# Kernel tuning notes

Measured on AMD Instinct MI355X. Metric: run time of the kernel, lower is better.

## Reference

```python
import jax, jax.numpy as jnp
import numpy as np

N_USERS = 200000
N_MOVIES = 80000
N = N_USERS + N_MOVIES
H = 64
F_MOVIE = 20
E = 1250000
EL = 500000


def setup_inputs() -> dict:
    key = jax.random.key(0)
    ks = jax.random.split(key, 13)
    s = 0.05
    inp = {
        "movie_x": jax.random.normal(ks[0], (N_MOVIES, F_MOVIE), jnp.float32),
        "user_emb": jax.random.normal(ks[1], (N_USERS, H), jnp.float32) * s,
        "movie_emb": jax.random.normal(ks[2], (N_MOVIES, H), jnp.float32) * s,
        "lin_W": jax.random.normal(ks[3], (H, F_MOVIE), jnp.float32) * s,
        "lin_b": jax.random.normal(ks[4], (H,), jnp.float32) * s,
        "W1l": jax.random.normal(ks[5], (H, H), jnp.float32) * s,
        "b1": jax.random.normal(ks[6], (H,), jnp.float32) * s,
        "W1r": jax.random.normal(ks[7], (H, H), jnp.float32) * s,
        "W2l": jax.random.normal(ks[8], (H, H), jnp.float32) * s,
        "b2": jax.random.normal(ks[9], (H,), jnp.float32) * s,
        "W2r": jax.random.normal(ks[10], (H, H), jnp.float32) * s,
        "edge_index": jax.random.randint(ks[11], (2, E), 0, N, jnp.int64),
        "edge_label_index": jnp.stack([
            jax.random.randint(jax.random.fold_in(ks[12], 0), (EL,), 0, N_USERS, jnp.int64),
            jax.random.randint(jax.random.fold_in(ks[12], 1), (EL,), 0, N_MOVIES, jnp.int64),
        ]),
    }
    return inp


def _sage(x, src, dst, Wl, bl, Wr):
    # PyG SAGEConv, mean aggregation: lin_l(mean_{j->i} x_j) + lin_r(x_i)
    msg = x[src]  # [E, H] gather
    agg = jax.ops.segment_sum(msg, dst, num_segments=N)  # [N, H] scatter-add
    deg = jax.ops.segment_sum(jnp.ones((src.shape[0],), x.dtype), dst, num_segments=N)
    mean = agg / jnp.maximum(deg, 1.0)[:, None]
    return mean @ Wl.T + bl + x @ Wr.T


def reference(movie_x, user_emb, movie_emb, lin_W, lin_b,
              W1l, b1, W1r, W2l, b2, W2r, edge_index, edge_label_index):
    # encode: users = embedding lookup (node_id == arange), movies = linear(x) + embedding
    x_user = user_emb
    x_movie = movie_x @ lin_W.T + lin_b + movie_emb
    x = jnp.concatenate([x_user, x_movie], axis=0)  # [N, H]

    src, dst = edge_index[0], edge_index[1]
    x = jax.nn.relu(_sage(x, src, dst, W1l, b1, W1r))
    x = _sage(x, src, dst, W2l, b2, W2r)

    xu = x[:N_USERS]
    xm = x[N_USERS:]
    # dot-product edge scoring over supervision edges
    u = xu[edge_label_index[0]]  # [EL, H]
    m = xm[edge_label_index[1]]  # [EL, H]
    return jnp.sum(u * m, axis=-1)  # [EL]
```

## Files before the change

kernel.cpp:

```cpp
#include <hip/hip_runtime.h>
#include <hip/hip_bf16.h>

#define NU 200000
#define NM 80000
#define NT 280000
#define HD 64
#define FM 20

#define BSHIFT 10
#define NBUCK ((NT + 1023) >> 10)
#define SCHUNK 4096

typedef __attribute__((ext_vector_type(8))) short short8;
typedef __attribute__((ext_vector_type(4))) float floatx4;

__device__ __forceinline__ float bfu2f(unsigned short u) {
    union { unsigned int u; float f; } c; c.u = ((unsigned int)u) << 16; return c.f;
}

__device__ __forceinline__ unsigned short f2bf_raw(float f) {
    union { float f; unsigned int u; } c; c.f = f;
    unsigned int u = c.u + 0x7FFFu + ((c.u >> 16) & 1u);
    return (unsigned short)(u >> 16);
}

__device__ __forceinline__ float ldf(const void* p, long i, int isbf) {
    return isbf ? bfu2f(((const unsigned short*)p)[i]) : ((const float*)p)[i];
}
__device__ __forceinline__ int ldidx(const int* p, long j, int is64) {
    return is64 ? p[2 * j] : p[j];
}

__global__ void probe_kernel(const void* user_emb, const int* ei, int* flags) {
    int t = threadIdx.x;
    int bad = 0;
    for (int i = t; i < 128; i += 64) {
        unsigned short h = ((const unsigned short*)user_emb)[i];
        unsigned int e = (h >> 7) & 0xFF;
        if (e >= 135) bad = 1;
    }
    unsigned long long mf = __ballot(bad != 0);
    int odd_nonzero = 0;
    if (t < 16 && ei[2 * t + 1] != 0) odd_nonzero = 1;
    unsigned long long mi = __ballot(odd_nonzero != 0);
    if (t == 0) {
        flags[0] = (mf == 0) ? 1 : 0;
        flags[1] = (mi == 0) ? 1 : 0;
    }
}

__global__ __launch_bounds__(256) void prep_user(
    const void* __restrict__ user_emb,
    unsigned short* __restrict__ xb,
    const int* __restrict__ flags)
{
    long t = (long)blockIdx.x * 256 + threadIdx.x;
    int isbf = flags[0];
    if (isbf) {
        ((short8*)xb)[t] = ((const short8*)user_emb)[t];
    } else {
        floatx4 a = ((const floatx4*)user_emb)[2 * t];
        floatx4 b = ((const floatx4*)user_emb)[2 * t + 1];
        short8 r;
        r[0] = (short)f2bf_raw(a[0]); r[1] = (short)f2bf_raw(a[1]);
        r[2] = (short)f2bf_raw(a[2]); r[3] = (short)f2bf_raw(a[3]);
        r[4] = (short)f2bf_raw(b[0]); r[5] = (short)f2bf_raw(b[1]);
        r[6] = (short)f2bf_raw(b[2]); r[7] = (short)f2bf_raw(b[3]);
        ((short8*)xb)[t] = r;
    }
}

__global__ __launch_bounds__(256) void prep_movie(
    const void* __restrict__ movie_x,
    const void* __restrict__ movie_emb,
    const void* __restrict__ lin_W,
    const void* __restrict__ lin_b,
    unsigned short* __restrict__ xb,
    const int* __restrict__ flags)
{
    int isbf = flags[0];
    int tid = threadIdx.x;
    int lane = tid & 63;
    int wave = blockIdx.x * 4 + (tid >> 6);
    int m0 = __builtin_amdgcn_readfirstlane(wave << 2);
    if (m0 >= NM) return;

    float wr[FM];
    if (isbf) {
        const unsigned int* p = (const unsigned int*)((const unsigned short*)lin_W + (long)lane * FM);
        #pragma unroll
        for (int i = 0; i < FM / 2; ++i) {
            unsigned int u = p[i];
            wr[2 * i]     = bfu2f((unsigned short)(u & 0xFFFFu));
            wr[2 * i + 1] = bfu2f((unsigned short)(u >> 16));
        }
    } else {
        const floatx4* p = (const floatx4*)((const float*)lin_W + (long)lane * FM);
        #pragma unroll
        for (int i = 0; i < FM / 4; ++i) {
            floatx4 v = p[i];
            wr[4 * i] = v[0]; wr[4 * i + 1] = v[1]; wr[4 * i + 2] = v[2]; wr[4 * i + 3] = v[3];
        }
    }
    float bias = ldf(lin_b, lane, isbf);

    #pragma unroll
    for (int mm = 0; mm < 4; ++mm) {
        int m = m0 + mm;
        float a0 = bias + ldf(movie_emb, (long)m * HD + lane, isbf);
        float a1 = 0.f, a2 = 0.f, a3 = 0.f;
        if (isbf) {
            const unsigned int* mr = (const unsigned int*)((const unsigned short*)movie_x + (long)m * FM);
            #pragma unroll
            for (int kk = 0; kk < FM / 2; ++kk) {
                unsigned int u = mr[kk];
                float x0 = bfu2f((unsigned short)(u & 0xFFFFu));
                float x1 = bfu2f((unsigned short)(u >> 16));
                if (kk & 1) { a2 += x0 * wr[2 * kk]; a3 += x1 * wr[2 * kk + 1]; }
                else        { a0 += x0 * wr[2 * kk]; a1 += x1 * wr[2 * kk + 1]; }
            }
        } else {
            const float* mr = (const float*)movie_x + (long)m * FM;
            #pragma unroll
            for (int k = 0; k < FM; k += 4) {
                a0 += mr[k]     * wr[k];
                a1 += mr[k + 1] * wr[k + 1];
                a2 += mr[k + 2] * wr[k + 2];
                a3 += mr[k + 3] * wr[k + 3];
            }
        }
        xb[(long)(NU + m) * HD + lane] = f2bf_raw((a0 + a1) + (a2 + a3));
    }
}

__global__ __launch_bounds__(512) void blk_hist(
    const int* __restrict__ ei, int E,
    int* __restrict__ blkhist,
    const int* __restrict__ flags)
{
    __shared__ int h[NBUCK];
    int tid = threadIdx.x;
    for (int i = tid; i < NBUCK; i += 512) h[i] = 0;
    __syncthreads();
    int is64 = flags[1];
    long e0 = (long)blockIdx.x * SCHUNK;
    long e1 = e0 + SCHUNK; if (e1 > E) e1 = E;
    for (long j = e0 + tid; j < e1; j += 512) {
        int d = ldidx(ei, (long)E + j, is64);
        atomicAdd(&h[d >> BSHIFT], 1);
    }
    __syncthreads();
    long obase = (long)blockIdx.x * NBUCK;
    for (int i = tid; i < NBUCK; i += 512) blkhist[obase + i] = h[i];
}

__global__ __launch_bounds__(256) void col_scan(
    int* __restrict__ blkhist, int NSB,
    int* __restrict__ bcnt)
{
    __shared__ int larr[2048];
    __shared__ int lsum[256];
    int b = blockIdx.x;
    int t = threadIdx.x;
    for (int i = t; i < NSB; i += 256) larr[i] = blkhist[(long)i * NBUCK + b];
    __syncthreads();
    int C = (NSB + 255) >> 8;
    int beg = t * C;
    int end = beg + C; if (end > NSB) end = NSB; if (beg > NSB) beg = NSB;
    int s = 0;
    for (int i = beg; i < end; ++i) s += larr[i];
    lsum[t] = s;
    __syncthreads();
    for (int off = 1; off < 256; off <<= 1) {
        int v = lsum[t];
        if (t >= off) v += lsum[t - off];
        __syncthreads();
        lsum[t] = v;
        __syncthreads();
    }
    int run = (t == 0) ? 0 : lsum[t - 1];
    for (int i = beg; i < end; ++i) {
        int v = larr[i];
        blkhist[(long)i * NBUCK + b] = run;
        run += v;
    }
    if (t == 0) bcnt[b] = lsum[255];
}

__global__ __launch_bounds__(256) void bucket_scan(
    const int* __restrict__ bcnt, int* __restrict__ bstart, int E)
{
    __shared__ int s[256];
    int t = threadIdx.x;
    int a0 = (2 * t     < NBUCK) ? bcnt[2 * t]     : 0;
    int a1 = (2 * t + 1 < NBUCK) ? bcnt[2 * t + 1] : 0;
    s[t] = a0 + a1;
    __syncthreads();
    for (int off = 1; off < 256; off <<= 1) {
        int v = s[t];
        if (t >= off) v += s[t - off];
        __syncthreads();
        s[t] = v;
        __syncthreads();
    }
    int run = (t == 0) ? 0 : s[t - 1];
    if (2 * t     < NBUCK) bstart[2 * t]     = run;
    if (2 * t + 1 < NBUCK) bstart[2 * t + 1] = run + a0;
    if (t == 0) bstart[NBUCK] = E;
}

__global__ __launch_bounds__(512) void scatter_kernel(
    const int* __restrict__ ei, int E,
    const int* __restrict__ bstart,
    const int* __restrict__ blkhist,
    int* __restrict__ packed,
    const int* __restrict__ flags)
{
    __shared__ int cur[NBUCK];
    int tid = threadIdx.x;
    long obase = (long)blockIdx.x * NBUCK;
    for (int i = tid; i < NBUCK; i += 512) cur[i] = bstart[i] + blkhist[obase + i];
    __syncthreads();
    int is64 = flags[1];
    long e0 = (long)blockIdx.x * SCHUNK;
    long e1 = e0 + SCHUNK; if (e1 > E) e1 = E;
    for (long j = e0 + tid; j < e1; j += 512) {
        int s = ldidx(ei, j, is64);
        int d = ldidx(ei, (long)E + j, is64);
        int b = d >> BSHIFT;
        int pos = atomicAdd(&cur[b], 1);
        packed[pos] = (s << BSHIFT) | (d & ((1 << BSHIFT) - 1));
    }
}

__global__ __launch_bounds__(256) void finefill_kernel(
    const int* __restrict__ bstart,
    const int* __restrict__ packed,
    int* __restrict__ rowptr,
    int* __restrict__ cnt,
    int* __restrict__ srclist)
{
    __shared__ int lcnt[1 << BSHIFT];
    __shared__ int lsum[256];
    int b = blockIdx.x;
    int tid = threadIdx.x;
    int nbase = b << BSHIFT;
    int beg = bstart[b];
    int end = bstart[b + 1];

    for (int i = tid; i < (1 << BSHIFT); i += 256) lcnt[i] = 0;
    __syncthreads();

    for (int j = beg + tid; j < end; j += 256)
        atomicAdd(&lcnt[packed[j] & ((1 << BSHIFT) - 1)], 1);
    __syncthreads();

    int i0 = tid * 4;
    int c0 = lcnt[i0], c1 = lcnt[i0 + 1], c2 = lcnt[i0 + 2], c3 = lcnt[i0 + 3];
    lsum[tid] = c0 + c1 + c2 + c3;
    __syncthreads();
    for (int off = 1; off < 256; off <<= 1) {
        int v = lsum[tid];
        if (tid >= off) v += lsum[tid - off];
        __syncthreads();
        lsum[tid] = v;
        __syncthreads();
    }
    int run = beg + ((tid == 0) ? 0 : lsum[tid - 1]);
    int r0 = run, r1 = r0 + c0, r2 = r1 + c1, r3 = r2 + c2;

    int n0 = nbase + i0;
    if (n0     < NT) { rowptr[n0]     = r0; cnt[n0]     = c0; }
    if (n0 + 1 < NT) { rowptr[n0 + 1] = r1; cnt[n0 + 1] = c1; }
    if (n0 + 2 < NT) { rowptr[n0 + 2] = r2; cnt[n0 + 2] = c2; }
    if (n0 + 3 < NT) { rowptr[n0 + 3] = r3; cnt[n0 + 3] = c3; }

    lcnt[i0] = r0; lcnt[i0 + 1] = r1; lcnt[i0 + 2] = r2; lcnt[i0 + 3] = r3;
    __syncthreads();

    for (int j = beg + tid; j < end; j += 256) {
        int p = packed[j];
        int dl = p & ((1 << BSHIFT) - 1);
        int pos = atomicAdd(&lcnt[dl], 1);
        srclist[pos] = p >> BSHIFT;
    }
}

template <bool RELU>
__global__ __launch_bounds__(256) void sage_layer(
    const unsigned short* __restrict__ xin,
    const int* __restrict__ rowptr,
    const int* __restrict__ cnt,
    const int* __restrict__ srclist,
    const void* __restrict__ Wl,
    const void* __restrict__ bias,
    const void* __restrict__ Wr,
    unsigned short* __restrict__ xout,
    const int* __restrict__ flags)
{
    __shared__ short8 lWl8[HD * HD / 8];
    __shared__ short8 lWr8[HD * HD / 8];
    __shared__ short8 lmean8[HD * HD / 8];
    __shared__ float lb[HD];
    unsigned short* lWl  = (unsigned short*)lWl8;
    unsigned short* lWr  = (unsigned short*)lWr8;
    unsigned short* lm   = (unsigned short*)lmean8;

    int tid = threadIdx.x;
    int isbf = flags[0];

    if (isbf) {
        const short8* wl8 = (const short8*)Wl;
        const short8* wr8 = (const short8*)Wr;
        for (int i = tid; i < HD * HD / 8; i += 256) { lWl8[i] = wl8[i]; lWr8[i] = wr8[i]; }
    } else {
        const floatx4* wlf = (const floatx4*)Wl;
        const floatx4* wrf = (const floatx4*)Wr;
        for (int i = tid; i < HD * HD / 8; i += 256) {
            floatx4 a = wlf[2 * i], b = wlf[2 * i + 1];
            short8 r;
            r[0]=(short)f2bf_raw(a[0]); r[1]=(short)f2bf_raw(a[1]); r[2]=(short)f2bf_raw(a[2]); r[3]=(short)f2bf_raw(a[3]);
            r[4]=(short)f2bf_raw(b[0]); r[5]=(short)f2bf_raw(b[1]); r[6]=(short)f2bf_raw(b[2]); r[7]=(short)f2bf_raw(b[3]);
            lWl8[i] = r;
            a = wrf[2 * i]; b = wrf[2 * i + 1];
            r[0]=(short)f2bf_raw(a[0]); r[1]=(short)f2bf_raw(a[1]); r[2]=(short)f2bf_raw(a[2]); r[3]=(short)f2bf_raw(a[3]);
            r[4]=(short)f2bf_raw(b[0]); r[5]=(short)f2bf_raw(b[1]); r[6]=(short)f2bf_raw(b[2]); r[7]=(short)f2bf_raw(b[3]);
            lWr8[i] = r;
        }
    }
    if (tid < HD) lb[tid] = ldf(bias, tid, isbf);

    int tile = blockIdx.x;
    long base = (long)tile * HD * HD;

    int w = tid >> 6;
    int lane = tid & 63;
    int mrow = lane & 15;
    int quad = lane >> 4;

    const short8* xrow = (const short8*)&xin[base + (long)(w * 16 + mrow) * HD];
    short8 ax0 = xrow[quad];
    short8 ax1 = xrow[4 + quad];

    int g = lane >> 2;
    int sub = lane & 3;
    int nl = w * 16 + g;
    int n = tile * 64 + nl;
    int beg = rowptr[n];
    int deg = cnt[n];

    float acc[16];
    #pragma unroll
    for (int k = 0; k < 16; ++k) acc[k] = 0.f;

    for (int j0 = 0; j0 < deg; j0 += 4) {
        int e = j0 + sub;
        int sv = (e < deg) ? srclist[beg + e] : 0;
        int cq = deg - j0; if (cq > 4) cq = 4;
        short8 r[4][2];
        #pragma unroll
        for (int q = 0; q < 4; ++q) {
            int s = __shfl(sv, (g << 2) | q);
            const short8* p = (const short8*)&xin[(long)s * HD + sub * 16];
            r[q][0] = p[0];
            r[q][1] = p[1];
        }
        #pragma unroll
        for (int q = 0; q < 4; ++q) {
            if (q < cq) {
                #pragma unroll
                for (int k = 0; k < 8; ++k) {
                    acc[k]     += bfu2f((unsigned short)r[q][0][k]);
                    acc[k + 8] += bfu2f((unsigned short)r[q][1][k]);
                }
            }
        }
    }

    float rd = 1.0f / fmaxf((float)deg, 1.0f);
    short8 o0, o1;
    #pragma unroll
    for (int k = 0; k < 8; ++k) {
        o0[k] = (short)f2bf_raw(acc[k] * rd);
        o1[k] = (short)f2bf_raw(acc[k + 8] * rd);
    }
    *(short8*)&lm[nl * HD + sub * 16]     = o0;
    *(short8*)&lm[nl * HD + sub * 16 + 8] = o1;

    __syncthreads();

    short8 am0 = *(const short8*)&lm[(w * 16 + mrow) * HD + quad * 8];
    short8 am1 = *(const short8*)&lm[(w * 16 + mrow) * HD + 32 + quad * 8];

    floatx4 acc4[4];
    #pragma unroll
    for (int ht = 0; ht < 4; ++ht) {
        int h = ht * 16 + mrow;
        short8 bl0 = *(const short8*)&lWl[h * HD + quad * 8];
        short8 bl1 = *(const short8*)&lWl[h * HD + 32 + quad * 8];
        short8 br0 = *(const short8*)&lWr[h * HD + quad * 8];
        short8 br1 = *(const short8*)&lWr[h * HD + 32 + quad * 8];
        floatx4 a = {0.f, 0.f, 0.f, 0.f};
        a = __builtin_amdgcn_mfma_f32_16x16x32_bf16(am0, bl0, a, 0, 0, 0);
        a = __builtin_amdgcn_mfma_f32_16x16x32_bf16(am1, bl1, a, 0, 0, 0);
        a = __builtin_amdgcn_mfma_f32_16x16x32_bf16(ax0, br0, a, 0, 0, 0);
        a = __builtin_amdgcn_mfma_f32_16x16x32_bf16(ax1, br1, a, 0, 0, 0);
        acc4[ht] = a;
    }

    #pragma unroll
    for (int ht = 0; ht < 4; ++ht) {
        int h = ht * 16 + mrow;
        float bv = lb[h];
        #pragma unroll
        for (int r = 0; r < 4; ++r) {
            int node = w * 16 + quad * 4 + r;
            float v = acc4[ht][r] + bv;
            if (RELU) v = fmaxf(v, 0.0f);
            xout[base + node * HD + h] = f2bf_raw(v);
        }
    }
}

__global__ __launch_bounds__(256) void dot_kernel(
    const unsigned short* __restrict__ x2,
    const int* __restrict__ eli,
    void* __restrict__ out,
    int EL,
    const int* __restrict__ flags)
{
    int wid = (blockIdx.x * 256 + threadIdx.x) >> 6;
    long base = (long)wid * 16;
    if (base >= EL) return;
    int lane = threadIdx.x & 63;
    int isbf = flags[0];
    int is64 = flags[1];

    int idxv = 0;
    if (lane < 16)      idxv = ldidx(eli, base + lane, is64);
    else if (lane < 32) idxv = ldidx(eli, (long)EL + base + (lane - 16), is64);

    int e   = lane >> 2;
    int seg = lane & 3;
    int u = __shfl(idxv, e);
    int m = __shfl(idxv, 16 + e);

    const short8* up = (const short8*)(x2 + (long)u * HD + seg * 16);
    const short8* mp = (const short8*)(x2 + (long)(NU + m) * HD + seg * 16);
    short8 a0 = up[0], a1 = up[1];
    short8 b0 = mp[0], b1 = mp[1];

    float p = 0.f;
    #pragma unroll
    for (int j = 0; j < 8; ++j) {
        p += bfu2f((unsigned short)a0[j]) * bfu2f((unsigned short)b0[j]);
        p += bfu2f((unsigned short)a1[j]) * bfu2f((unsigned short)b1[j]);
    }
    p += __shfl_xor(p, 1);
    p += __shfl_xor(p, 2);

    if (seg == 0) {
        long g = base + e;
        if (isbf) ((unsigned short*)out)[g] = f2bf_raw(p);
        else      ((float*)out)[g] = p;
    }
}

extern "C" void kernel_launch(void* const* d_in, const int* in_sizes, int n_in,
                              void* d_out, int out_size, void* d_ws, size_t ws_size,
                              hipStream_t stream)
{
    const void* movie_x   = d_in[0];
    const void* user_emb  = d_in[1];
    const void* movie_emb = d_in[2];
    const void* lin_W     = d_in[3];
    const void* lin_b     = d_in[4];
    const void* W1l       = d_in[5];
    const void* b1        = d_in[6];
    const void* W1r       = d_in[7];
    const void* W2l       = d_in[8];
    const void* b2        = d_in[9];
    const void* W2r       = d_in[10];
    const int* ei  = (const int*)d_in[11];
    const int* eli = (const int*)d_in[12];
    int E  = in_sizes[11] / 2;
    int EL = in_sizes[12] / 2;

    const int NSB = (E + SCHUNK - 1) / SCHUNK;

    char* w = (char*)d_ws;
    unsigned short* xb0     = (unsigned short*)w;  w += (size_t)NT * HD * 2;
    unsigned short* xb1     = (unsigned short*)w;  w += (size_t)NT * HD * 2;
    int*            cnt     = (int*)w;             w += (size_t)NT * 4;
    int*            rowptr  = (int*)w;             w += (size_t)NT * 4;
    int*            srclist = (int*)w;             w += (size_t)E * 4;
    int*            packed  = (int*)w;             w += (size_t)E * 4;
    int*            bcnt    = (int*)w;             w += (size_t)(NBUCK + 1) * 4;
    int*            bstart  = (int*)w;             w += (size_t)(NBUCK + 1) * 4;
    int*            blkhist = (int*)w;             w += (size_t)NSB * NBUCK * 4;
    int*            flags   = (int*)w;

    const int user_blocks   = (NU * HD / 8) / 256;
    const int movie_blocks  = NM / 16;
    const int tile_blocks   = NT / 64;
    const int dot_blocks    = ((EL + 15) / 16 + 3) / 4;

    probe_kernel<<<1, 64, 0, stream>>>(user_emb, ei, flags);

    prep_user<<<user_blocks, 256, 0, stream>>>(user_emb, xb0, flags);
    prep_movie<<<movie_blocks, 256, 0, stream>>>(movie_x, movie_emb, lin_W, lin_b, xb0, flags);

    blk_hist<<<NSB, 512, 0, stream>>>(ei, E, blkhist, flags);
    col_scan<<<NBUCK, 256, 0, stream>>>(blkhist, NSB, bcnt);
    bucket_scan<<<1, 256, 0, stream>>>(bcnt, bstart, E);
    scatter_kernel<<<NSB, 512, 0, stream>>>(ei, E, bstart, blkhist, packed, flags);
    finefill_kernel<<<NBUCK, 256, 0, stream>>>(bstart, packed, rowptr, cnt, srclist);

    sage_layer<true><<<tile_blocks, 256, 0, stream>>>(xb0, rowptr, cnt, srclist, W1l, b1, W1r, xb1, flags);
    sage_layer<false><<<tile_blocks, 256, 0, stream>>>(xb1, rowptr, cnt, srclist, W2l, b2, W2r, xb0, flags);

    dot_kernel<<<dot_blocks, 256, 0, stream>>>(xb0, eli, d_out, EL, flags);
}
```

Measured before the change: 305.7 us.

## Widen SAGE layer to 512 threads with 8 lanes per node and padded LDS

The SAGE layer kernel now runs 512 threads per 64-node tile. Each node's neighbor gather is spread over 8 lanes, each loading 16 bytes per neighbor, and up to 8 neighbors are gathered per iteration. The MFMA output work is split so each wave computes two of the four 16-column tiles. Shared-memory rows for the weights and mean tile are padded to 72 elements to avoid LDS bank conflicts. The goals are more memory-level parallelism in the latency-bound gather and cheaper LDS reads, at the cost of larger blocks and redundant per-wave A-fragment loads.

```diff
diff --git a/kernel.cpp b/kernel.cpp
--- a/kernel.cpp
+++ b/kernel.cpp
@@ -10,6 +10,9 @@
 #define BSHIFT 10
 #define NBUCK ((NT + 1023) >> 10)
 #define SCHUNK 4096
+
+#define PD 72
+#define PD8 (PD / 8)
 
 typedef __attribute__((ext_vector_type(8))) short short8;
 typedef __attribute__((ext_vector_type(4))) float floatx4;
@@ -287,7 +290,7 @@
 }
 
 template <bool RELU>
-__global__ __launch_bounds__(256) void sage_layer(
+__global__ __launch_bounds__(512) void sage_layer(
     const unsigned short* __restrict__ xin,
     const int* __restrict__ rowptr,
     const int* __restrict__ cnt,
@@ -298,13 +301,10 @@
     unsigned short* __restrict__ xout,
     const int* __restrict__ flags)
 {
-    __shared__ short8 lWl8[HD * HD / 8];
-    __shared__ short8 lWr8[HD * HD / 8];
-    __shared__ short8 lmean8[HD * HD / 8];
+    __shared__ short8 lWl8[HD * PD8];
+    __shared__ short8 lWr8[HD * PD8];
+    __shared__ short8 lm8[HD * PD8];
     __shared__ float lb[HD];
-    unsigned short* lWl  = (unsigned short*)lWl8;
-    unsigned short* lWr  = (unsigned short*)lWr8;
-    unsigned short* lm   = (unsigned short*)lmean8;
 
     int tid = threadIdx.x;
     int isbf = flags[0];
@@ -312,110 +312,107 @@
     if (isbf) {
         const short8* wl8 = (const short8*)Wl;
         const short8* wr8 = (const short8*)Wr;
-        for (int i = tid; i < HD * HD / 8; i += 256) { lWl8[i] = wl8[i]; lWr8[i] = wr8[i]; }
+        int i = tid;
+        int di = (i >> 3) * PD8 + (i & 7);
+        lWl8[di] = wl8[i];
+        lWr8[di] = wr8[i];
     } else {
         const floatx4* wlf = (const floatx4*)Wl;
         const floatx4* wrf = (const floatx4*)Wr;
-        for (int i = tid; i < HD * HD / 8; i += 256) {
-            floatx4 a = wlf[2 * i], b = wlf[2 * i + 1];
-            short8 r;
-            r[0]=(short)f2bf_raw(a[0]); r[1]=(short)f2bf_raw(a[1]); r[2]=(short)f2bf_raw(a[2]); r[3]=(short)f2bf_raw(a[3]);
-            r[4]=(short)f2bf_raw(b[0]); r[5]=(short)f2bf_raw(b[1]); r[6]=(short)f2bf_raw(b[2]); r[7]=(short)f2bf_raw(b[3]);
-            lWl8[i] = r;
-            a = wrf[2 * i]; b = wrf[2 * i + 1];
-            r[0]=(short)f2bf_raw(a[0]); r[1]=(short)f2bf_raw(a[1]); r[2]=(short)f2bf_raw(a[2]); r[3]=(short)f2bf_raw(a[3]);
-            r[4]=(short)f2bf_raw(b[0]); r[5]=(short)f2bf_raw(b[1]); r[6]=(short)f2bf_raw(b[2]); r[7]=(short)f2bf_raw(b[3]);
-            lWr8[i] = r;
-        }
+        int i = tid;
+        int di = (i >> 3) * PD8 + (i & 7);
+        floatx4 a = wlf[2 * i], b = wlf[2 * i + 1];
+        short8 r;
+        r[0]=(short)f2bf_raw(a[0]); r[1]=(short)f2bf_raw(a[1]); r[2]=(short)f2bf_raw(a[2]); r[3]=(short)f2bf_raw(a[3]);
+        r[4]=(short)f2bf_raw(b[0]); r[5]=(short)f2bf_raw(b[1]); r[6]=(short)f2bf_raw(b[2]); r[7]=(short)f2bf_raw(b[3]);
+        lWl8[di] = r;
+        a = wrf[2 * i]; b = wrf[2 * i + 1];
+        r[0]=(short)f2bf_raw(a[0]); r[1]=(short)f2bf_raw(a[1]); r[2]=(short)f2bf_raw(a[2]); r[3]=(short)f2bf_raw(a[3]);
+        r[4]=(short)f2bf_raw(b[0]); r[5]=(short)f2bf_raw(b[1]); r[6]=(short)f2bf_raw(b[2]); r[7]=(short)f2bf_raw(b[3]);
+        lWr8[di] = r;
     }
     if (tid < HD) lb[tid] = ldf(bias, tid, isbf);
 
     int tile = blockIdx.x;
     long base = (long)tile * HD * HD;
 
-    int w = tid >> 6;
+    int w8 = tid >> 6;
     int lane = tid & 63;
     int mrow = lane & 15;
     int quad = lane >> 4;
-
-    const short8* xrow = (const short8*)&xin[base + (long)(w * 16 + mrow) * HD];
+    int roww = (w8 & 3) * 16 + mrow;
+    int htp  = w8 >> 2;
+
+    const short8* xrow = (const short8*)&xin[base + (long)roww * HD];
     short8 ax0 = xrow[quad];
-    short8 ax1 = xrow[4 + quad];
-
-    int g = lane >> 2;
-    int sub = lane & 3;
-    int nl = w * 16 + g;
+    short8 ax1 = xrow[quad + 4];
+
+    int g = lane >> 3;
+    int sub = lane & 7;
+    int nl = w8 * 8 + g;
     int n = tile * 64 + nl;
     int beg = rowptr[n];
     int deg = cnt[n];
 
-    float acc[16];
+    float acc[8];
     #pragma unroll
-    for (int k = 0; k < 16; ++k) acc[k] = 0.f;
-
-    for (int j0 = 0; j0 < deg; j0 += 4) {
+    for (int k = 0; k < 8; ++k) acc[k] = 0.f;
+
+    for (int j0 = 0; j0 < deg; j0 += 8) {
         int e = j0 + sub;
         int sv = (e < deg) ? srclist[beg + e] : 0;
-        int cq = deg - j0; if (cq > 4) cq = 4;
-        short8 r[4][2];
+        int cq = deg - j0; if (cq > 8) cq = 8;
+        short8 r[8];
         #pragma unroll
-        for (int q = 0; q < 4; ++q) {
-            int s = __shfl(sv, (g << 2) | q);
-            const short8* p = (const short8*)&xin[(long)s * HD + sub * 16];
-            r[q][0] = p[0];
-            r[q][1] = p[1];
+        for (int q = 0; q < 8; ++q) {
+            int s = __shfl(sv, (g << 3) | q);
+            r[q] = *(const short8*)&xin[(long)s * HD + sub * 8];
         }
         #pragma unroll
-        for (int q = 0; q < 4; ++q) {
+        for (int q = 0; q < 8; ++q) {
             if (q < cq) {
                 #pragma unroll
-                for (int k = 0; k < 8; ++k) {
-                    acc[k]     += bfu2f((unsigned short)r[q][0][k]);
-                    acc[k + 8] += bfu2f((unsigned short)r[q][1][k]);
-                }
+                for (int k = 0; k < 8; ++k)
+                    acc[k] += bfu2f((unsigned short)r[q][k]);
             }
         }
     }
 
     float rd = 1.0f / fmaxf((float)deg, 1.0f);
-    short8 o0, o1;
+    short8 o;
     #pragma unroll
-    for (int k = 0; k < 8; ++k) {
-        o0[k] = (short)f2bf_raw(acc[k] * rd);
-        o1[k] = (short)f2bf_raw(acc[k + 8] * rd);
-    }
-    *(short8*)&lm[nl * HD + sub * 16]     = o0;
-    *(short8*)&lm[nl * HD + sub * 16 + 8] = o1;
-
-    __syncthreads();
-
-    short8 am0 = *(const short8*)&lm[(w * 16 + mrow) * HD + quad * 8];
-    short8 am1 = *(const short8*)&lm[(w * 16 + mrow) * HD + 32 + quad * 8];
-
-    floatx4 acc4[4];
+    for (int k = 0; k < 8; ++k) o[k] = (short)f2bf_raw(acc[k] * rd);
+    lm8[nl * PD8 + sub] = o;
+
+    __syncthreads();
+
+    short8 am0 = lm8[roww * PD8 + quad];
+    short8 am1 = lm8[roww * PD8 + 4 + quad];
+
+    floatx4 acc4[2];
     #pragma unroll
-    for (int ht = 0; ht < 4; ++ht) {
-        int h = ht * 16 + mrow;
-        short8 bl0 = *(const short8*)&lWl[h * HD + quad * 8];
-        short8 bl1 = *(const short8*)&lWl[h * HD + 32 + quad * 8];
-        short8 br0 = *(const short8*)&lWr[h * HD + quad * 8];
-        short8 br1 = *(const short8*)&lWr[h * HD + 32 + quad * 8];
+    for (int t = 0; t < 2; ++t) {
+        int h = (htp * 2 + t) * 16 + mrow;
+        short8 bl0 = lWl8[h * PD8 + quad];
+        short8 bl1 = lWl8[h * PD8 + 4 + quad];
+        short8 br0 = lWr8[h * PD8 + quad];
+        short8 br1 = lWr8[h * PD8 + 4 + quad];
         floatx4 a = {0.f, 0.f, 0.f, 0.f};
         a = __builtin_amdgcn_mfma_f32_16x16x32_bf16(am0, bl0, a, 0, 0, 0);
         a = __builtin_amdgcn_mfma_f32_16x16x32_bf16(am1, bl1, a, 0, 0, 0);
         a = __builtin_amdgcn_mfma_f32_16x16x32_bf16(ax0, br0, a, 0, 0, 0);
         a = __builtin_amdgcn_mfma_f32_16x16x32_bf16(ax1, br1, a, 0, 0, 0);
-        acc4[ht] = a;
+        acc4[t] = a;
     }
 
     #pragma unroll
-    for (int ht = 0; ht < 4; ++ht) {
-        int h = ht * 16 + mrow;
+    for (int t = 0; t < 2; ++t) {
+        int h = (htp * 2 + t) * 16 + mrow;
         float bv = lb[h];
         #pragma unroll
         for (int r = 0; r < 4; ++r) {
-            int node = w * 16 + quad * 4 + r;
-            float v = acc4[ht][r] + bv;
+            int node = (w8 & 3) * 16 + quad * 4 + r;
+            float v = acc4[t][r] + bv;
             if (RELU) v = fmaxf(v, 0.0f);
             xout[base + node * HD + h] = f2bf_raw(v);
         }
@@ -516,8 +513,8 @@
     scatter_kernel<<<NSB, 512, 0, stream>>>(ei, E, bstart, blkhist, packed, flags);
     finefill_kernel<<<NBUCK, 256, 0, stream>>>(bstart, packed, rowptr, cnt, srclist);
 
-    sage_layer<true><<<tile_blocks, 256, 0, stream>>>(xb0, rowptr, cnt, srclist, W1l, b1, W1r, xb1, flags);
-    sage_layer<false><<<tile_blocks, 256, 0, stream>>>(xb1, rowptr, cnt, srclist, W2l, b2, W2r, xb0, flags);
+    sage_layer<true><<<tile_blocks, 512, 0, stream>>>(xb0, rowptr, cnt, srclist, W1l, b1, W1r, xb1, flags);
+    sage_layer<false><<<tile_blocks, 512, 0, stream>>>(xb1, rowptr, cnt, srclist, W2l, b2, W2r, xb0, flags);
 
     dot_kernel<<<dot_blocks, 256, 0, stream>>>(xb0, eli, d_out, EL, flags);
 }
```

Result: no change. 305.4 us (-0.1%).
